# Optimization experiments

Measured on AMD Instinct MI355X. Metric: run time of the kernel, lower is better.

## Reference

```python
import jax, jax.numpy as jnp
import numpy as np

N = 20000      # nodes
E = 320000     # edges (avg degree 16)
F_IN = 768
DIMS = [(768, 1536), (1536, 768), (768, 384), (384, 256), (256, 5)]


def setup_inputs() -> dict:
    key = jax.random.key(0)
    ks = jax.random.split(key, 2 + 3 * len(DIMS))
    inp = {
        'x': jax.random.normal(ks[0], (N, F_IN), dtype=jnp.float32),
        'edge_index': jax.random.randint(ks[1], (2, E), 0, N, dtype=jnp.int64),
    }
    for li, (fi, fo) in enumerate(DIMS):
        s = 1.0 / np.sqrt(fi)
        inp[f'Wl{li+1}'] = jax.random.uniform(ks[2 + 3 * li], (fi, fo), jnp.float32, -s, s)
        inp[f'Wr{li+1}'] = jax.random.uniform(ks[3 + 3 * li], (fi, fo), jnp.float32, -s, s)
        inp[f'b{li+1}'] = jax.random.uniform(ks[4 + 3 * li], (fo,), jnp.float32, -s, s)
    return inp


def _sage_conv(x, src, dst, deg_inv, Wl, Wr, b):
    # mean aggregate neighbor features, then linear (mean commutes with linear,
    # matching PyG SAGEConv which aggregates x_j then applies lin_l)
    agg = jax.ops.segment_sum(x[src], dst, num_segments=N) * deg_inv  # [N, F_in]
    return agg @ Wl + x @ Wr + b


def reference(x, edge_index,
              Wl1, Wr1, b1, Wl2, Wr2, b2, Wl3, Wr3, b3,
              Wl4, Wr4, b4, Wl5, Wr5, b5):
    src, dst = edge_index[0], edge_index[1]
    deg = jax.ops.segment_sum(jnp.ones((E,), jnp.float32), dst, num_segments=N)
    deg_inv = (1.0 / jnp.maximum(deg, 1.0))[:, None]  # clamp like PyG mean aggr

    h = jax.nn.relu(_sage_conv(x, src, dst, deg_inv, Wl1, Wr1, b1))
    h = jax.nn.relu(_sage_conv(h, src, dst, deg_inv, Wl2, Wr2, b2))
    h = jax.nn.relu(_sage_conv(h, src, dst, deg_inv, Wl3, Wr3, b3))
    h = jax.nn.relu(_sage_conv(h, src, dst, deg_inv, Wl4, Wr4, b4))  # [N, 256]
    out = _sage_conv(h, src, dst, deg_inv, Wl5, Wr5, b5)             # [N, 5]
    return (h, out)
```

## Files before the change

kernel.cpp:

```cpp
#include <hip/hip_runtime.h>
#include <stdint.h>

typedef __attribute__((ext_vector_type(8))) short short8;
typedef __attribute__((ext_vector_type(4))) float f32x4;

__device__ __forceinline__ float bf2f(unsigned short s) {
  return __uint_as_float(((unsigned)s) << 16);
}
__device__ __forceinline__ unsigned short f2bf(float f) {
  unsigned u = __float_as_uint(f);
  u += 0x7fffu + ((u >> 16) & 1u);
  return (unsigned short)(u >> 16);
}

__global__ void gs_count_deg(const int* __restrict__ dst, int* __restrict__ cnt, int E) {
  int e = blockIdx.x * 256 + threadIdx.x;
  if (e < E) atomicAdd(&cnt[dst[e]], 1);
}

__global__ void gs_scanA(const int* __restrict__ cnt, int* __restrict__ rp,
                         int* __restrict__ bsum, int n) {
  __shared__ int sm[256];
  const int b = blockIdx.x, t = threadIdx.x;
  const int base = b * 1024 + t * 4;
  int v[4]; int s = 0;
#pragma unroll
  for (int i = 0; i < 4; ++i) { v[i] = (base + i < n) ? cnt[base + i] : 0; s += v[i]; }
  sm[t] = s;
  __syncthreads();
  for (int off = 1; off < 256; off <<= 1) {
    int x = (t >= off) ? sm[t - off] : 0;
    __syncthreads();
    sm[t] += x;
    __syncthreads();
  }
  int run = sm[t] - s;
#pragma unroll
  for (int i = 0; i < 4; ++i) { if (base + i < n) rp[base + i] = run; run += v[i]; }
  if (t == 255) bsum[b] = sm[255];
}

__global__ void gs_scanB(int* bsum, int nb) {
  if (threadIdx.x == 0 && blockIdx.x == 0) {
    int run = 0;
    for (int i = 0; i < nb; ++i) { int v = bsum[i]; bsum[i] = run; run += v; }
    bsum[nb] = run;
  }
}

__global__ void gs_scanC(int* __restrict__ rp, int* __restrict__ cur,
                         const int* __restrict__ bsum, int n, int nb) {
  int i = blockIdx.x * 256 + threadIdx.x;
  if (i < n) {
    int v = rp[i] + bsum[i >> 10];
    rp[i] = v;
    cur[i] = v;
  }
  if (i == n) rp[n] = bsum[nb];
}

__global__ void gs_fill_csr(const int* __restrict__ src, const int* __restrict__ dst,
                            int* __restrict__ cur, int* __restrict__ col, int E) {
  int e = blockIdx.x * 256 + threadIdx.x;
  if (e < E) {
    int pos = atomicAdd(&cur[dst[e]], 1);
    col[pos] = src[e];
  }
}

__global__ void gs_f32_to_bf16(const float* __restrict__ in, unsigned short* __restrict__ out, int n4) {
  int i = blockIdx.x * 256 + threadIdx.x;
  if (i < n4) {
    float4 f = ((const float4*)in)[i];
    ushort4 o;
    o.x = f2bf(f.x); o.y = f2bf(f.y); o.z = f2bf(f.z); o.w = f2bf(f.w);
    ((ushort4*)out)[i] = o;
  }
}

struct TP { const float* W; unsigned short* WT; int K, F; };
struct TP8 { TP t[8]; };

__global__ void gs_tpack8(TP8 args) {
  const TP a = args.t[blockIdx.z];
  const int k0 = blockIdx.x * 32, f0 = blockIdx.y * 32;
  if (k0 >= a.K || f0 >= a.F) return;
  __shared__ float t[32][33];
  const int tx = threadIdx.x, ty = threadIdx.y;
#pragma unroll
  for (int r = ty; r < 32; r += 8) {
    int k = k0 + r, f = f0 + tx;
    t[r][tx] = (k < a.K && f < a.F) ? a.W[(size_t)k * a.F + f] : 0.f;
  }
  __syncthreads();
#pragma unroll
  for (int r = ty; r < 32; r += 8) {
    int f = f0 + r, k = k0 + tx;
    if (f < a.F && k < a.K) a.WT[(size_t)f * a.K + k] = f2bf(t[tx][r]);
  }
}

__global__ __launch_bounds__(64)
void gs_agg_slice(const unsigned short* __restrict__ C, int ldc, int zoff,
                  const int* __restrict__ rp, const int* __restrict__ col,
                  const float* __restrict__ bias,
                  unsigned short* __restrict__ hout, float* __restrict__ fout,
                  int F, int relu) {
  const int v = blockIdx.x;
  const int cc = blockIdx.y * 128 + 2 * threadIdx.x;
  const int l = threadIdx.x;
  const int s0 = rp[v], s1 = rp[v + 1];
  const float inv = 1.0f / (float)max(s1 - s0, 1);
  float a0 = 0.f, a1 = 0.f;
  __shared__ int nb[64];
  for (int base = s0; base < s1; base += 64) {
    int m = min(s1 - base, 64);
    __syncthreads();
    if (l < m) nb[l] = col[base + l];
    __syncthreads();
    int j = 0;
    for (; j + 4 <= m; j += 4) {
      ushort2 u0 = *(const ushort2*)(C + (size_t)nb[j + 0] * ldc + cc);
      ushort2 u1 = *(const ushort2*)(C + (size_t)nb[j + 1] * ldc + cc);
      ushort2 u2 = *(const ushort2*)(C + (size_t)nb[j + 2] * ldc + cc);
      ushort2 u3 = *(const ushort2*)(C + (size_t)nb[j + 3] * ldc + cc);
      a0 += bf2f(u0.x) + bf2f(u1.x) + bf2f(u2.x) + bf2f(u3.x);
      a1 += bf2f(u0.y) + bf2f(u1.y) + bf2f(u2.y) + bf2f(u3.y);
    }
    for (; j < m; ++j) {
      ushort2 u = *(const ushort2*)(C + (size_t)nb[j] * ldc + cc);
      a0 += bf2f(u.x); a1 += bf2f(u.y);
    }
  }
  float o0 = a0 * inv, o1 = a1 * inv;
  if (zoff >= 0) {
    ushort2 u = *(const ushort2*)(C + (size_t)v * ldc + zoff + cc);
    o0 += bf2f(u.x); o1 += bf2f(u.y);
  }
  if (bias) { o0 += bias[cc]; o1 += bias[cc + 1]; }
  if (relu) { o0 = fmaxf(o0, 0.f); o1 = fmaxf(o1, 0.f); }
  if (hout) {
    ushort2 u; u.x = f2bf(o0); u.y = f2bf(o1);
    *(ushort2*)(hout + (size_t)v * F + cc) = u;
  }
  if (fout) *(float2*)(fout + (size_t)v * F + cc) = make_float2(o0, o1);
}

__global__ __launch_bounds__(256)
void gs_gemm(const unsigned short* __restrict__ A1, const unsigned short* __restrict__ A2,
             const unsigned short* __restrict__ B1, const unsigned short* __restrict__ B2,
             const float* __restrict__ bias, unsigned short* __restrict__ Hout,
             int M, int Nn, int K, int doRelu, int Mt, int Nt) {
  __shared__ unsigned short lA[128 * 64];
  __shared__ unsigned short lB[128 * 64];
  const int tid = threadIdx.x;
  const int wid = tid >> 6;
  const int lane = tid & 63;

  const int MG = 8;
  const int per = MG * Nt;
  const int g = blockIdx.x / per;
  const int rem = blockIdx.x - g * per;
  const int gsz = min(MG, Mt - g * MG);
  const int nIdx = rem / gsz;
  const int mIdx = g * MG + (rem - nIdx * gsz);
  const int bM = mIdx * 128;
  const int bN = nIdx * 128;
  const int wM = (wid >> 1) * 64;
  const int wN = (wid & 1) * 64;

  f32x4 acc[4][4];
#pragma unroll
  for (int i = 0; i < 4; ++i)
#pragma unroll
    for (int j = 0; j < 4; ++j) acc[i][j] = (f32x4){0.f, 0.f, 0.f, 0.f};

  const int mrow = wM + (lane & 15);
  const int nrow = wN + (lane & 15);
  const int q = lane >> 4;
  const int swz = lane & 7;
  const int srow = wid * 8 + (lane >> 3);
  const int sc = (lane & 7) ^ (lane >> 3);
  const int npass = A2 ? 2 : 1;

  for (int pass = 0; pass < npass; ++pass) {
    const unsigned short* Ap = pass ? A2 : A1;
    const unsigned short* Bp = pass ? B2 : B1;
    for (int k0 = 0; k0 < K; k0 += 64) {
#pragma unroll
      for (int r = 0; r < 4; ++r) {
        int row = r * 32 + srow;
        int ga = bM + row;
        if (ga >= M) ga = M - 1;
        const unsigned short* gpA = Ap + (size_t)ga * K + k0 + sc * 8;
        const unsigned short* gpB = Bp + (size_t)(bN + row) * K + k0 + sc * 8;
        unsigned lo = (unsigned)(r * 32 + wid * 8) * 128;
        __builtin_amdgcn_global_load_lds(
            (const __attribute__((address_space(1))) unsigned int*)gpA,
            (__attribute__((address_space(3))) unsigned int*)((char*)lA + lo), 16, 0, 0);
        __builtin_amdgcn_global_load_lds(
            (const __attribute__((address_space(1))) unsigned int*)gpB,
            (__attribute__((address_space(3))) unsigned int*)((char*)lB + lo), 16, 0, 0);
      }
      __syncthreads();
#pragma unroll
      for (int s = 0; s < 2; ++s) {
        const int cofs = ((s * 4 + q) ^ swz) * 8;
        short8 aF[4], bF[4];
#pragma unroll
        for (int i = 0; i < 4; ++i) {
          aF[i] = *(const short8*)&lA[(mrow + i * 16) * 64 + cofs];
          bF[i] = *(const short8*)&lB[(nrow + i * 16) * 64 + cofs];
        }
#pragma unroll
        for (int i = 0; i < 4; ++i)
#pragma unroll
          for (int j = 0; j < 4; ++j)
            acc[i][j] = __builtin_amdgcn_mfma_f32_16x16x32_bf16(aF[i], bF[j], acc[i][j], 0, 0, 0);
      }
      __syncthreads();
    }
  }

  const int rbase = bM + wM + (lane >> 4) * 4;
#pragma unroll
  for (int i = 0; i < 4; ++i) {
#pragma unroll
    for (int r = 0; r < 4; ++r) {
      int row = rbase + i * 16 + r;
      if (row >= M) continue;
#pragma unroll
      for (int j = 0; j < 4; ++j) {
        int colN = bN + wN + j * 16 + (lane & 15);
        float v = acc[i][j][r];
        if (bias) v += bias[colN];
        if (doRelu) v = fmaxf(v, 0.f);
        Hout[(size_t)row * Nn + colN] = f2bf(v);
      }
    }
  }
}

__global__ __launch_bounds__(64)
void gs_l5dot(const unsigned short* __restrict__ h4, const float* __restrict__ Wl,
              const float* __restrict__ Wr, float* __restrict__ yz) {
  __shared__ float sW[2560];
  const int v = blockIdx.x;
  const int l = threadIdx.x;
  for (int i = l; i < 2560; i += 64) sW[i] = (i < 1280) ? Wl[i] : Wr[i - 1280];
  __syncthreads();
  ushort4 u = ((const ushort4*)(h4 + (size_t)v * 256))[l];
  float hv[4] = {bf2f(u.x), bf2f(u.y), bf2f(u.z), bf2f(u.w)};
  float acc[10];
#pragma unroll
  for (int n = 0; n < 10; ++n) acc[n] = 0.f;
#pragma unroll
  for (int t = 0; t < 4; ++t) {
    int k = 4 * l + t;
#pragma unroll
    for (int n = 0; n < 5; ++n) {
      acc[n] += hv[t] * sW[k * 5 + n];
      acc[5 + n] += hv[t] * sW[1280 + k * 5 + n];
    }
  }
#pragma unroll
  for (int n = 0; n < 10; ++n)
    for (int off = 32; off > 0; off >>= 1) acc[n] += __shfl_down(acc[n], off, 64);
  if (l == 0) {
#pragma unroll
    for (int n = 0; n < 10; ++n) yz[(size_t)v * 10 + n] = acc[n];
  }
}

__global__ __launch_bounds__(64)
void gs_l5agg(const float* __restrict__ yz, const int* __restrict__ rp,
              const int* __restrict__ col, const float* __restrict__ b,
              float* __restrict__ out) {
  const int v = blockIdx.x;
  const int l = threadIdx.x;
  const int s0 = rp[v], s1 = rp[v + 1];
  const float inv = 1.0f / (float)max(s1 - s0, 1);
  float acc[5] = {0.f, 0.f, 0.f, 0.f, 0.f};
  for (int e = s0 + l; e < s1; e += 64) {
    const float* yr = yz + (size_t)col[e] * 10;
#pragma unroll
    for (int n = 0; n < 5; ++n) acc[n] += yr[n];
  }
#pragma unroll
  for (int n = 0; n < 5; ++n)
    for (int off = 32; off > 0; off >>= 1) acc[n] += __shfl_down(acc[n], off, 64);
  if (l == 0) {
#pragma unroll
    for (int n = 0; n < 5; ++n)
      out[(size_t)v * 5 + n] = acc[n] * inv + yz[(size_t)v * 10 + 5 + n] + b[n];
  }
}

extern "C" void kernel_launch(void* const* d_in, const int* in_sizes, int n_in,
                              void* d_out, int out_size, void* d_ws, size_t ws_size,
                              hipStream_t stream) {
  const float* x = (const float*)d_in[0];
  const int* ei = (const int*)d_in[1];
  const int N = in_sizes[0] / 768;
  const int E = in_sizes[1] / 2;
  const int* src = ei;
  const int* dst = ei + E;

  const float* Wl[5];
  const float* Wr[5];
  const float* bb[5];
  for (int l = 0; l < 5; ++l) {
    Wl[l] = (const float*)d_in[2 + 3 * l];
    Wr[l] = (const float*)d_in[3 + 3 * l];
    bb[l] = (const float*)d_in[4 + 3 * l];
  }

  char* w = (char*)d_ws;
  size_t off = 0;
  auto take = [&](size_t bytes) -> char* {
    char* p = w + off;
    off = (off + bytes + 255) & ~(size_t)255;
    return p;
  };
  unsigned short* ar1 = (unsigned short*)take((size_t)N * 768 * 2);
  unsigned short* ar2 = (unsigned short*)take((size_t)N * 768 * 2);
  unsigned short* ar3 = (unsigned short*)take((size_t)N * 1536 * 2);
  unsigned short* C2  = (unsigned short*)take((size_t)N * 1536 * 2);
  int* cnt  = (int*)take((size_t)N * 4);
  int* rp   = (int*)take((size_t)(N + 1) * 4);
  int* cur  = (int*)take((size_t)N * 4);
  int* col  = (int*)take((size_t)E * 4);
  const int nbChunks = (N + 1023) / 1024;
  int* bsum = (int*)take((size_t)(nbChunks + 1) * 4);
  unsigned short* WT1l = (unsigned short*)take((size_t)1536 * 768 * 2);
  unsigned short* WT1r = (unsigned short*)take((size_t)1536 * 768 * 2);
  unsigned short* WT2  = (unsigned short*)take((size_t)1536 * 1536 * 2);
  unsigned short* WT3  = (unsigned short*)take((size_t)768 * 768 * 2);
  unsigned short* WT4  = (unsigned short*)take((size_t)512 * 384 * 2);

  unsigned short* xb   = ar1;
  unsigned short* C3   = ar1;
  unsigned short* aggb = ar2;
  unsigned short* h2   = ar2;
  unsigned short* h1   = ar3;
  unsigned short* C4   = ar3;
  unsigned short* h3   = ar3 + (size_t)N * 512;
  unsigned short* h4   = ar3 + (size_t)N * (512 + 384);
  float*          yz5  = (float*)(ar3 + (size_t)N * (512 + 384 + 256));

  const int M = N;
  const int Mt = (M + 127) / 128;

  hipMemsetAsync(cnt, 0, (size_t)N * 4, stream);
  gs_count_deg<<<(E + 255) / 256, 256, 0, stream>>>(dst, cnt, E);
  gs_scanA<<<nbChunks, 256, 0, stream>>>(cnt, rp, bsum, N);
  gs_scanB<<<1, 64, 0, stream>>>(bsum, nbChunks);
  gs_scanC<<<(N + 256) / 256, 256, 0, stream>>>(rp, cur, bsum, N, nbChunks);
  gs_fill_csr<<<(E + 255) / 256, 256, 0, stream>>>(src, dst, cur, col, E);

  gs_f32_to_bf16<<<((N * 768 / 4) + 255) / 256, 256, 0, stream>>>(x, xb, N * 768 / 4);
  TP8 tp;
  tp.t[0] = {Wl[0], WT1l, 768, 1536};
  tp.t[1] = {Wr[0], WT1r, 768, 1536};
  tp.t[2] = {Wl[1], WT2, 1536, 768};
  tp.t[3] = {Wr[1], WT2 + (size_t)768 * 1536, 1536, 768};
  tp.t[4] = {Wl[2], WT3, 768, 384};
  tp.t[5] = {Wr[2], WT3 + (size_t)384 * 768, 768, 384};
  tp.t[6] = {Wl[3], WT4, 384, 256};
  tp.t[7] = {Wr[3], WT4 + (size_t)256 * 384, 384, 256};
  gs_tpack8<<<dim3(48, 48, 8), dim3(32, 8), 0, stream>>>(tp);

  float* houtF = (float*)d_out;
  float* out5  = (float*)d_out + (size_t)N * 256;

  gs_agg_slice<<<dim3(N, 6), 64, 0, stream>>>(xb, 768, -1, rp, col, nullptr, aggb, nullptr, 768, 0);
  gs_gemm<<<Mt * 12, 256, 0, stream>>>(aggb, xb, WT1l, WT1r, bb[0], h1, M, 1536, 768, 1, Mt, 12);

  gs_gemm<<<Mt * 12, 256, 0, stream>>>(h1, nullptr, WT2, nullptr, nullptr, C2, M, 1536, 1536, 0, Mt, 12);
  gs_agg_slice<<<dim3(N, 6), 64, 0, stream>>>(C2, 1536, 768, rp, col, bb[1], h2, nullptr, 768, 1);

  gs_gemm<<<Mt * 6, 256, 0, stream>>>(h2, nullptr, WT3, nullptr, nullptr, C3, M, 768, 768, 0, Mt, 6);
  gs_agg_slice<<<dim3(N, 3), 64, 0, stream>>>(C3, 768, 384, rp, col, bb[2], h3, nullptr, 384, 1);

  gs_gemm<<<Mt * 4, 256, 0, stream>>>(h3, nullptr, WT4, nullptr, nullptr, C4, M, 512, 384, 0, Mt, 4);
  gs_agg_slice<<<dim3(N, 2), 64, 0, stream>>>(C4, 512, 256, rp, col, bb[3], h4, houtF, 256, 1);

  gs_l5dot<<<N, 64, 0, stream>>>(h4, Wl[4], Wr[4], yz5);
  gs_l5agg<<<N, 64, 0, stream>>>(yz5, rp, col, bb[4], out5);
}
```

Before: 699.3 us.

## Rewrite GEMM as 256x256 tile, 8-wave, double-buffered pipelined kernel

The bf16 MFMA GEMM moves from a 128x128 tile with 4 waves and a single LDS buffer to a 256x256 tile with 8 waves. LDS is double-buffered and split into half-tiles, and global-to-LDS loads for later k-steps are interleaved with MFMA phases using explicit barriers, waitcnt and setprio. The goal is to hide global load latency behind compute and raise data reuse per block. In exchange it uses much more LDS (128KB per block) and registers. Fewer, larger tiles also waste work on the partial last M tile and may leave some CUs idle for the smaller layers.

```diff
diff --git a/kernel.cpp b/kernel.cpp
--- a/kernel.cpp
+++ b/kernel.cpp
@@ -146,13 +146,59 @@
   if (fout) *(float2*)(fout + (size_t)v * F + cc) = make_float2(o0, o1);
 }
 
-__global__ __launch_bounds__(256)
+#define GLL(SRC, DST) __builtin_amdgcn_global_load_lds(                        \
+    (const __attribute__((address_space(1))) unsigned int*)(SRC),              \
+    (__attribute__((address_space(3))) unsigned int*)(DST), 16, 0, 0)
+
+#define PHASE(T, MH, NH, ST_T, ST_B, ST_H, DO_VM)                              \
+  {                                                                            \
+    const int buf_ = (T) & 1;                                                  \
+    const unsigned short* Ab_ = &lA[buf_][MH][0];                              \
+    const unsigned short* Bb_ = &lB[buf_][NH][0];                              \
+    short8 aF_[4][2], bF_[2][2];                                               \
+    _Pragma("unroll")                                                          \
+    for (int fi = 0; fi < 4; ++fi) {                                           \
+      int lra = wMl + fi * 16;                                                 \
+      _Pragma("unroll")                                                        \
+      for (int ks = 0; ks < 2; ++ks) {                                         \
+        int ch = (ks * 4 + qk) ^ (lra & 7);                                    \
+        aF_[fi][ks] = *(const short8*)&Ab_[lra * 64 + ch * 8];                 \
+      }                                                                        \
+    }                                                                          \
+    _Pragma("unroll")                                                          \
+    for (int fj = 0; fj < 2; ++fj) {                                           \
+      int lrb = wNl + fj * 16;                                                 \
+      _Pragma("unroll")                                                        \
+      for (int ks = 0; ks < 2; ++ks) {                                         \
+        int ch = (ks * 4 + qk) ^ (lrb & 7);                                    \
+        bF_[fj][ks] = *(const short8*)&Bb_[lrb * 64 + ch * 8];                 \
+      }                                                                        \
+    }                                                                          \
+    STAGE(ST_T, ST_B, ST_H);                                                   \
+    __builtin_amdgcn_s_barrier();                                              \
+    asm volatile("s_waitcnt lgkmcnt(0)" ::: "memory");                         \
+    __builtin_amdgcn_sched_barrier(0);                                         \
+    __builtin_amdgcn_s_setprio(1);                                             \
+    _Pragma("unroll")                                                          \
+    for (int fi = 0; fi < 4; ++fi)                                             \
+      _Pragma("unroll")                                                        \
+      for (int fj = 0; fj < 2; ++fj)                                           \
+        _Pragma("unroll")                                                      \
+        for (int ks = 0; ks < 2; ++ks)                                         \
+          acc[MH][fi][NH][fj] = __builtin_amdgcn_mfma_f32_16x16x32_bf16(       \
+              aF_[fi][ks], bF_[fj][ks], acc[MH][fi][NH][fj], 0, 0, 0);         \
+    __builtin_amdgcn_s_setprio(0);                                             \
+    if (DO_VM) asm volatile("s_waitcnt vmcnt(4)" ::: "memory");                \
+    __builtin_amdgcn_s_barrier();                                              \
+  }
+
+__global__ __launch_bounds__(512, 2)
 void gs_gemm(const unsigned short* __restrict__ A1, const unsigned short* __restrict__ A2,
              const unsigned short* __restrict__ B1, const unsigned short* __restrict__ B2,
              const float* __restrict__ bias, unsigned short* __restrict__ Hout,
              int M, int Nn, int K, int doRelu, int Mt, int Nt) {
-  __shared__ unsigned short lA[128 * 64];
-  __shared__ unsigned short lB[128 * 64];
+  __shared__ unsigned short lA[2][2][8192];
+  __shared__ unsigned short lB[2][2][8192];
   const int tid = threadIdx.x;
   const int wid = tid >> 6;
   const int lane = tid & 63;
@@ -164,81 +210,94 @@
   const int gsz = min(MG, Mt - g * MG);
   const int nIdx = rem / gsz;
   const int mIdx = g * MG + (rem - nIdx * gsz);
-  const int bM = mIdx * 128;
-  const int bN = nIdx * 128;
-  const int wM = (wid >> 1) * 64;
-  const int wN = (wid & 1) * 64;
-
-  f32x4 acc[4][4];
-#pragma unroll
-  for (int i = 0; i < 4; ++i)
-#pragma unroll
-    for (int j = 0; j < 4; ++j) acc[i][j] = (f32x4){0.f, 0.f, 0.f, 0.f};
-
-  const int mrow = wM + (lane & 15);
-  const int nrow = wN + (lane & 15);
-  const int q = lane >> 4;
-  const int swz = lane & 7;
-  const int srow = wid * 8 + (lane >> 3);
-  const int sc = (lane & 7) ^ (lane >> 3);
-  const int npass = A2 ? 2 : 1;
-
-  for (int pass = 0; pass < npass; ++pass) {
-    const unsigned short* Ap = pass ? A2 : A1;
-    const unsigned short* Bp = pass ? B2 : B1;
-    for (int k0 = 0; k0 < K; k0 += 64) {
+  const int bM = mIdx * 256;
+  const int bN = nIdx * 256;
+
+  const int wM_ = wid >> 2;
+  const int wN_ = wid & 3;
+  const int qk  = lane >> 4;
+  const int wMl = wM_ * 64 + (lane & 15);
+  const int wNl = wN_ * 32 + (lane & 15);
+
+  const int lr  = tid >> 3;
+  const int swk = ((tid & 7) ^ (lr & 7)) * 8;
+  const int rB0 = (lr >> 5) * 64 + (lr & 31);
+
+  const int kt = K / 64;
+  const int nt = A2 ? 2 * kt : kt;
+  const int NI = nt / 2;
+
+  f32x4 acc[2][4][2][2];
+#pragma unroll
+  for (int a = 0; a < 2; ++a)
+#pragma unroll
+    for (int b = 0; b < 4; ++b)
+#pragma unroll
+      for (int c = 0; c < 2; ++c)
+#pragma unroll
+        for (int d = 0; d < 2; ++d) acc[a][b][c][d] = (f32x4){0.f, 0.f, 0.f, 0.f};
+
+  auto STAGE = [&](int t, int isB, int h) {
+    const int tc = (t < nt) ? t : (nt - 1);
+    const int pass = (tc >= kt) ? 1 : 0;
+    const int k0 = (tc - pass * kt) * 64;
+    const int buf = t & 1;
+    if (!isB) {
+      const unsigned short* Ap = pass ? A2 : A1;
+      int r1 = bM + h * 64 + lr;
+      int r2 = r1 + 128;
+      if (r1 >= M) r1 = M - 1;
+      if (r2 >= M) r2 = M - 1;
+      char* d = (char*)&lA[buf][h][0] + wid * 1024;
+      GLL(Ap + (size_t)r1 * K + k0 + swk, d);
+      GLL(Ap + (size_t)r2 * K + k0 + swk, d + 8192);
+    } else {
+      const unsigned short* Bp = pass ? B2 : B1;
+      int r1 = bN + h * 32 + rB0;
+      char* d = (char*)&lB[buf][h][0] + wid * 1024;
+      GLL(Bp + (size_t)r1 * K + k0 + swk, d);
+      GLL(Bp + (size_t)(r1 + 128) * K + k0 + swk, d + 8192);
+    }
+  };
+
+  STAGE(0, 0, 0); STAGE(0, 1, 0); STAGE(0, 0, 1); STAGE(0, 1, 1);
+  STAGE(1, 0, 0); STAGE(1, 1, 0);
+  asm volatile("s_waitcnt vmcnt(4)" ::: "memory");
+  __builtin_amdgcn_s_barrier();
+
+  for (int i = 0; i < NI; ++i) {
+    const int t0 = 2 * i, t1 = t0 + 1, t2 = t0 + 2, t3 = t0 + 3;
+    PHASE(t0, 0, 0, t1, 0, 1, 0)
+    PHASE(t0, 0, 1, t1, 1, 1, 0)
+    PHASE(t0, 1, 0, t2, 0, 0, 0)
+    PHASE(t0, 1, 1, t2, 1, 0, 1)
+    PHASE(t1, 0, 0, t2, 0, 1, 0)
+    PHASE(t1, 0, 1, t2, 1, 1, 0)
+    PHASE(t1, 1, 0, t3, 0, 0, 0)
+    PHASE(t1, 1, 1, t3, 1, 0, 1)
+  }
+
+#pragma unroll
+  for (int mh = 0; mh < 2; ++mh)
+#pragma unroll
+    for (int fi = 0; fi < 4; ++fi) {
+      const int row0 = bM + wM_ * 128 + mh * 64 + fi * 16 + (lane >> 4) * 4;
 #pragma unroll
       for (int r = 0; r < 4; ++r) {
-        int row = r * 32 + srow;
-        int ga = bM + row;
-        if (ga >= M) ga = M - 1;
-        const unsigned short* gpA = Ap + (size_t)ga * K + k0 + sc * 8;
-        const unsigned short* gpB = Bp + (size_t)(bN + row) * K + k0 + sc * 8;
-        unsigned lo = (unsigned)(r * 32 + wid * 8) * 128;
-        __builtin_amdgcn_global_load_lds(
-            (const __attribute__((address_space(1))) unsigned int*)gpA,
-            (__attribute__((address_space(3))) unsigned int*)((char*)lA + lo), 16, 0, 0);
-        __builtin_amdgcn_global_load_lds(
-            (const __attribute__((address_space(1))) unsigned int*)gpB,
-            (__attribute__((address_space(3))) unsigned int*)((char*)lB + lo), 16, 0, 0);
-      }
-      __syncthreads();
-#pragma unroll
-      for (int s = 0; s < 2; ++s) {
-        const int cofs = ((s * 4 + q) ^ swz) * 8;
-        short8 aF[4], bF[4];
-#pragma unroll
-        for (int i = 0; i < 4; ++i) {
-          aF[i] = *(const short8*)&lA[(mrow + i * 16) * 64 + cofs];
-          bF[i] = *(const short8*)&lB[(nrow + i * 16) * 64 + cofs];
-        }
-#pragma unroll
-        for (int i = 0; i < 4; ++i)
-#pragma unroll
-          for (int j = 0; j < 4; ++j)
-            acc[i][j] = __builtin_amdgcn_mfma_f32_16x16x32_bf16(aF[i], bF[j], acc[i][j], 0, 0, 0);
-      }
-      __syncthreads();
-    }
-  }
-
-  const int rbase = bM + wM + (lane >> 4) * 4;
-#pragma unroll
-  for (int i = 0; i < 4; ++i) {
-#pragma unroll
-    for (int r = 0; r < 4; ++r) {
-      int row = rbase + i * 16 + r;
-      if (row >= M) continue;
-#pragma unroll
-      for (int j = 0; j < 4; ++j) {
-        int colN = bN + wN + j * 16 + (lane & 15);
-        float v = acc[i][j][r];
-        if (bias) v += bias[colN];
-        if (doRelu) v = fmaxf(v, 0.f);
-        Hout[(size_t)row * Nn + colN] = f2bf(v);
+        const int row = row0 + r;
+        if (row >= M) continue;
+#pragma unroll
+        for (int nh = 0; nh < 2; ++nh)
+#pragma unroll
+          for (int fj = 0; fj < 2; ++fj) {
+            const int colN = bN + wN_ * 64 + nh * 32 + fj * 16 + (lane & 15);
+            float v = acc[mh][fi][nh][fj][r];
+            if (bias) v += bias[colN];
+            if (doRelu) v = fmaxf(v, 0.f);
+            Hout[(size_t)row * Nn + colN] = f2bf(v);
+          }
       }
     }
-  }
 }
 
 __global__ __launch_bounds__(64)
@@ -349,7 +408,7 @@
   float*          yz5  = (float*)(ar3 + (size_t)N * (512 + 384 + 256));
 
   const int M = N;
-  const int Mt = (M + 127) / 128;
+  const int Mt = (M + 255) / 256;
 
   hipMemsetAsync(cnt, 0, (size_t)N * 4, stream);
   gs_count_deg<<<(E + 255) / 256, 256, 0, stream>>>(dst, cnt, E);
@@ -374,15 +433,15 @@
   float* out5  = (float*)d_out + (size_t)N * 256;
 
   gs_agg_slice<<<dim3(N, 6), 64, 0, stream>>>(xb, 768, -1, rp, col, nullptr, aggb, nullptr, 768, 0);
-  gs_gemm<<<Mt * 12, 256, 0, stream>>>(aggb, xb, WT1l, WT1r, bb[0], h1, M, 1536, 768, 1, Mt, 12);
-
-  gs_gemm<<<Mt * 12, 256, 0, stream>>>(h1, nullptr, WT2, nullptr, nullptr, C2, M, 1536, 1536, 0, Mt, 12);
+  gs_gemm<<<Mt * 6, 512, 0, stream>>>(aggb, xb, WT1l, WT1r, bb[0], h1, M, 1536, 768, 1, Mt, 6);
+
+  gs_gemm<<<Mt * 6, 512, 0, stream>>>(h1, nullptr, WT2, nullptr, nullptr, C2, M, 1536, 1536, 0, Mt, 6);
   gs_agg_slice<<<dim3(N, 6), 64, 0, stream>>>(C2, 1536, 768, rp, col, bb[1], h2, nullptr, 768, 1);
 
-  gs_gemm<<<Mt * 6, 256, 0, stream>>>(h2, nullptr, WT3, nullptr, nullptr, C3, M, 768, 768, 0, Mt, 6);
+  gs_gemm<<<Mt * 3, 512, 0, stream>>>(h2, nullptr, WT3, nullptr, nullptr, C3, M, 768, 768, 0, Mt, 3);
   gs_agg_slice<<<dim3(N, 3), 64, 0, stream>>>(C3, 768, 384, rp, col, bb[2], h3, nullptr, 384, 1);
 
-  gs_gemm<<<Mt * 4, 256, 0, stream>>>(h3, nullptr, WT4, nullptr, nullptr, C4, M, 512, 384, 0, Mt, 4);
+  gs_gemm<<<Mt * 2, 512, 0, stream>>>(h3, nullptr, WT4, nullptr, nullptr, C4, M, 512, 384, 0, Mt, 2);
   gs_agg_slice<<<dim3(N, 2), 64, 0, stream>>>(C4, 512, 256, rp, col, bb[3], h4, houtF, 256, 1);
 
   gs_l5dot<<<N, 64, 0, stream>>>(h4, Wl[4], Wr[4], yz5);
```

New measurement: 735.3 us. +5.1%, slower.
